# Optimization experiments

Measured on AMD Instinct MI355X. Metric: run time of the kernel, lower is better.

## Reference

```python
import jax, jax.numpy as jnp
import numpy as np

EPS = 1e-6  # LayerNorm eps (added to std, matching torch code)
H = 4       # n_heads
B, D, N, DFF = 8, 512, 1024, 1024


def layer_norm(x, g, b):
    # torch: a_2 * (x - mean) / (std + eps) + b_2, std unbiased (ddof=1)
    m = x.mean(-1, keepdims=True)
    s = x.std(-1, ddof=1, keepdims=True)
    return g * (x - m) / (s + EPS) + b


def mha(q, k, v, W, b):
    # W: [4, d, d] (in->out), b: [4, d]; heads H, d_k = d // H
    Bq, Nq, d = q.shape
    dk = d // H

    def proj(x, i):
        return (x @ W[i] + b[i]).reshape(Bq, -1, H, dk).transpose(0, 2, 1, 3)

    Q, K, V = proj(q, 0), proj(k, 1), proj(v, 2)
    scores = jnp.einsum('bhqd,bhkd->bhqk', Q, K) / np.sqrt(dk).astype(np.float32)
    p = jax.nn.softmax(scores, axis=-1)
    o = jnp.einsum('bhqk,bhkd->bhqd', p, V).transpose(0, 2, 1, 3).reshape(Bq, -1, d)
    return o @ W[3] + b[3]


def ffn(x, w1, b1, w2, b2):
    return jax.nn.relu(x @ w1 + b1) @ w2 + b2


def encoder(x, aw, ab, fw1, fb1, fw2, fb2, lg, lb):
    x = x + mha(layer_norm(x, lg[0], lb[0]), layer_norm(x, lg[0], lb[0]), layer_norm(x, lg[0], lb[0]), aw, ab)
    x = x + ffn(layer_norm(x, lg[1], lb[1]), fw1, fb1, fw2, fb2)
    return layer_norm(x, lg[2], lb[2])


def decoder(x, mem, sw, sb, cw, cb, fw1, fb1, fw2, fb2, lg, lb):
    h0 = layer_norm(x, lg[0], lb[0])
    x = x + mha(h0, h0, h0, sw, sb)
    h1 = layer_norm(x, lg[1], lb[1])
    x = x + mha(h1, mem, mem, cw, cb)
    x = x + ffn(layer_norm(x, lg[2], lb[2]), fw1, fb1, fw2, fb2)
    return layer_norm(x, lg[3], lb[3])


def model(src, tgt, p):
    # src, tgt: [B, N, D]
    mem = encoder(src, p['enc_attn_w'], p['enc_attn_b'], p['enc_ff_w1'], p['enc_ff_b1'],
                  p['enc_ff_w2'], p['enc_ff_b2'], p['enc_ln_g'], p['enc_ln_b'])
    return decoder(tgt, mem, p['dec_sa_w'], p['dec_sa_b'], p['dec_ca_w'], p['dec_ca_b'],
                   p['dec_ff_w1'], p['dec_ff_b1'], p['dec_ff_w2'], p['dec_ff_b2'],
                   p['dec_ln_g'], p['dec_ln_b'])


def setup_inputs() -> dict:
    key = jax.random.key(0)
    ks = jax.random.split(key, 12)
    sc = 0.02
    return {
        'src': jax.random.normal(ks[0], (B, D, N), jnp.float32),
        'tgt': jax.random.normal(ks[1], (B, D, N), jnp.float32),
        'enc_attn_w': jax.random.normal(ks[2], (4, D, D), jnp.float32) * sc,
        'enc_attn_b': jnp.zeros((4, D), jnp.float32),
        'enc_ff_w1': jax.random.normal(ks[3], (D, DFF), jnp.float32) * sc,
        'enc_ff_b1': jnp.zeros((DFF,), jnp.float32),
        'enc_ff_w2': jax.random.normal(ks[4], (DFF, D), jnp.float32) * sc,
        'enc_ff_b2': jnp.zeros((D,), jnp.float32),
        'enc_ln_g': jnp.ones((3, D), jnp.float32),
        'enc_ln_b': jnp.zeros((3, D), jnp.float32),
        'dec_sa_w': jax.random.normal(ks[5], (4, D, D), jnp.float32) * sc,
        'dec_sa_b': jnp.zeros((4, D), jnp.float32),
        'dec_ca_w': jax.random.normal(ks[6], (4, D, D), jnp.float32) * sc,
        'dec_ca_b': jnp.zeros((4, D), jnp.float32),
        'dec_ff_w1': jax.random.normal(ks[7], (D, DFF), jnp.float32) * sc,
        'dec_ff_b1': jnp.zeros((DFF,), jnp.float32),
        'dec_ff_w2': jax.random.normal(ks[8], (DFF, D), jnp.float32) * sc,
        'dec_ff_b2': jnp.zeros((D,), jnp.float32),
        'dec_ln_g': jnp.ones((4, D), jnp.float32),
        'dec_ln_b': jnp.zeros((4, D), jnp.float32),
    }


def reference(src, tgt, enc_attn_w, enc_attn_b, enc_ff_w1, enc_ff_b1, enc_ff_w2, enc_ff_b2,
              enc_ln_g, enc_ln_b, dec_sa_w, dec_sa_b, dec_ca_w, dec_ca_b,
              dec_ff_w1, dec_ff_b1, dec_ff_w2, dec_ff_b2, dec_ln_g, dec_ln_b):
    p = dict(enc_attn_w=enc_attn_w, enc_attn_b=enc_attn_b, enc_ff_w1=enc_ff_w1,
             enc_ff_b1=enc_ff_b1, enc_ff_w2=enc_ff_w2, enc_ff_b2=enc_ff_b2,
             enc_ln_g=enc_ln_g, enc_ln_b=enc_ln_b, dec_sa_w=dec_sa_w, dec_sa_b=dec_sa_b,
             dec_ca_w=dec_ca_w, dec_ca_b=dec_ca_b, dec_ff_w1=dec_ff_w1, dec_ff_b1=dec_ff_b1,
             dec_ff_w2=dec_ff_w2, dec_ff_b2=dec_ff_b2, dec_ln_g=dec_ln_g, dec_ln_b=dec_ln_b)
    s = src.transpose(0, 2, 1)  # [B, N, D]
    t = tgt.transpose(0, 2, 1)
    tgt_embedding = model(s, t, p).transpose(0, 2, 1)  # [B, D, N]
    src_embedding = model(t, s, p).transpose(0, 2, 1)
    return (src_embedding, tgt_embedding)
```

## Files before the change

### kernel.cpp

```cpp
#include <hip/hip_runtime.h>

#define BB 8
#define NN 1024
#define DD 512
#define DFFK 1024
#define HH 4
#define RR (BB * NN)
#define MM (2 * RR)

typedef unsigned short u16;
typedef u16 u16x8 __attribute__((ext_vector_type(8)));
typedef float f32x4 __attribute__((ext_vector_type(4)));
typedef __bf16 bf16x8 __attribute__((ext_vector_type(8)));

__device__ __forceinline__ u16 f32_to_bf16(float f) {
  unsigned int u = __builtin_bit_cast(unsigned int, f);
  unsigned int r = u + 0x7FFFu + ((u >> 16) & 1u);
  return (u16)(r >> 16);
}

__device__ __forceinline__ f32x4 mfma16(u16x8 a, u16x8 b, f32x4 c) {
  return __builtin_amdgcn_mfma_f32_16x16x32_bf16(
      __builtin_bit_cast(bf16x8, a), __builtin_bit_cast(bf16x8, b), c, 0, 0, 0);
}

__device__ __forceinline__ void gl16(u16* lds, const u16* g) {
  __builtin_amdgcn_global_load_lds(
      (const __attribute__((address_space(1))) unsigned int*)g,
      (__attribute__((address_space(3))) unsigned int*)lds, 16, 0, 0);
}

__global__ __launch_bounds__(256) void wconv_kernel(const float* __restrict__ W,
                                                    u16* __restrict__ Wt, int K, int N2, int nmat) {
  int idx = blockIdx.x * 256 + threadIdx.x;
  if (idx >= nmat * K * N2) return;
  int mat = idx / (K * N2), rem = idx % (K * N2);
  int k = rem % K, n = rem / K;
  Wt[(size_t)mat * K * N2 + (size_t)n * K + k] =
      f32_to_bf16(W[(size_t)mat * K * N2 + (size_t)k * N2 + n]);
}

__global__ __launch_bounds__(256) void transpose_kernel(const float* __restrict__ in,
                                                        float* __restrict__ out, int R_, int C_) {
  __shared__ float t[32][33];
  int bx = blockIdx.x * 32, by = blockIdx.y * 32;
  size_t zoff = (size_t)blockIdx.z * R_ * C_;
  const float* ip = in + zoff;
  float* op = out + zoff;
  int tx = threadIdx.x, ty = threadIdx.y;
#pragma unroll
  for (int i = 0; i < 32; i += 8)
    t[ty + i][tx] = ip[(size_t)(by + ty + i) * C_ + bx + tx];
  __syncthreads();
#pragma unroll
  for (int i = 0; i < 32; i += 8)
    op[(size_t)(bx + ty + i) * R_ + by + tx] = t[tx][ty + i];
}

__global__ __launch_bounds__(256) void out_trans_kernel(const float* __restrict__ in,
                                                        float* __restrict__ outA,
                                                        float* __restrict__ outB) {
  __shared__ float t[32][33];
  int z = blockIdx.z;
  int dx = blockIdx.x * 32;
  int sy = blockIdx.y * 32;
  int tx = threadIdx.x, ty = threadIdx.y;
  const float* ip = in + (size_t)z * NN * DD;
#pragma unroll
  for (int i = 0; i < 32; i += 8)
    t[ty + i][tx] = ip[(size_t)(sy + ty + i) * DD + dx + tx];
  __syncthreads();
  float* dst = (z < BB) ? (outA + (size_t)z * DD * NN) : (outB + (size_t)(z - BB) * DD * NN);
#pragma unroll
  for (int i = 0; i < 32; i += 8)
    dst[(size_t)(dx + ty + i) * NN + sy + tx] = t[tx][ty + i];
}

__global__ __launch_bounds__(256) void vtrans_kernel(const u16* __restrict__ V, int vstride,
                                                     u16* __restrict__ Vt) {
  __shared__ u16 t[32][33];
  int z = blockIdx.z;
  int b = z >> 2, h = z & 3;
  int sx = blockIdx.x * 32;
  int dy = blockIdx.y * 32;
  int tx = threadIdx.x, ty = threadIdx.y;
  const u16* ip = V + (size_t)b * NN * vstride + h * 128 + dy;
#pragma unroll
  for (int i = 0; i < 32; i += 8)
    t[ty + i][tx] = ip[(size_t)(sx + ty + i) * vstride + tx];
  __syncthreads();
  u16* op = Vt + ((size_t)z * 128 + dy) * NN + sx;
#pragma unroll
  for (int i = 0; i < 32; i += 8)
    op[(size_t)(ty + i) * NN + tx] = t[tx][ty + i];
}

template <int OUTBF>
__global__ __launch_bounds__(256) void ln_kernel(const float* __restrict__ x0,
                                                 const float* __restrict__ x1,
                                                 const float* __restrict__ g,
                                                 const float* __restrict__ bb,
                                                 void* __restrict__ out) {
  int l = threadIdx.x & 63, w = threadIdx.x >> 6;
  size_t row = (size_t)blockIdx.x * 4 + w;
  const float* xr = (row < RR) ? (x0 + row * DD) : (x1 + (row - RR) * DD);
  float4 v0 = *(const float4*)(xr + l * 8);
  float4 v1 = *(const float4*)(xr + l * 8 + 4);
  float sum = v0.x + v0.y + v0.z + v0.w + v1.x + v1.y + v1.z + v1.w;
  float sq = v0.x * v0.x + v0.y * v0.y + v0.z * v0.z + v0.w * v0.w +
             v1.x * v1.x + v1.y * v1.y + v1.z * v1.z + v1.w * v1.w;
#pragma unroll
  for (int o = 1; o < 64; o <<= 1) {
    sum += __shfl_xor(sum, o);
    sq += __shfl_xor(sq, o);
  }
  float mean = sum * (1.0f / DD);
  float var = fmaxf((sq - (float)DD * mean * mean) * (1.0f / (DD - 1)), 0.0f);
  float inv = 1.0f / (sqrtf(var) + 1e-6f);
  float4 g0 = *(const float4*)(g + l * 8), g1 = *(const float4*)(g + l * 8 + 4);
  float4 b0 = *(const float4*)(bb + l * 8), b1 = *(const float4*)(bb + l * 8 + 4);
  float xs[8] = {v0.x, v0.y, v0.z, v0.w, v1.x, v1.y, v1.z, v1.w};
  float gs[8] = {g0.x, g0.y, g0.z, g0.w, g1.x, g1.y, g1.z, g1.w};
  float bs[8] = {b0.x, b0.y, b0.z, b0.w, b1.x, b1.y, b1.z, b1.w};
  float y[8];
#pragma unroll
  for (int j = 0; j < 8; j++) y[j] = (xs[j] - mean) * inv * gs[j] + bs[j];
  if (OUTBF) {
    u16x8 o8;
#pragma unroll
    for (int j = 0; j < 8; j++) o8[j] = f32_to_bf16(y[j]);
    *(u16x8*)((u16*)out + row * DD + l * 8) = o8;
  } else {
    float4 o0 = {y[0], y[1], y[2], y[3]};
    float4 o1 = {y[4], y[5], y[6], y[7]};
    *(float4*)((float*)out + row * DD + l * 8) = o0;
    *(float4*)((float*)out + row * DD + l * 8 + 4) = o1;
  }
}

template <bool RELU, bool OUT_BF16, bool HAS_RES>
__global__ __launch_bounds__(512) void gemm_bt(const u16* __restrict__ A, int lda,
                                               const u16* __restrict__ Bt,
                                               const float* __restrict__ bias,
                                               const float* res0, const float* res1,
                                               void* Cout, int ldc,
                                               int N2, int Kd) {
  __shared__ u16 sA[2][1024 * 8];
  __shared__ u16 sB[2][512 * 8];
  int tid = threadIdx.x;
  int l = tid & 63, w = tid >> 6;
  int wm = (w >> 1) * 64, wn = (w & 1) * 64;
  int m0 = blockIdx.x * 256, n0 = blockIdx.y * 128;
  f32x4 acc[4][4] = {};

  auto stage = [&](int buf, int k0) {
#pragma unroll
    for (int is = 0; is < 2; is++) {
      int slot = is * 512 + w * 64 + l;
      int chunk = slot >> 8, row = slot & 255;
      gl16(&sA[buf][(size_t)(is * 512 + w * 64) * 8],
           A + (size_t)(m0 + row) * lda + k0 + chunk * 8);
    }
    {
      int slot = w * 64 + l;
      int chunk = slot >> 7, row = slot & 127;
      gl16(&sB[buf][(size_t)(w * 64) * 8],
           Bt + (size_t)(n0 + row) * Kd + k0 + chunk * 8);
    }
  };
  stage(0, 0);
  int buf = 0;
  for (int k0 = 0; k0 < Kd; k0 += 32) {
    __syncthreads();
    if (k0 + 32 < Kd) stage(buf ^ 1, k0 + 32);
    u16x8 af[4], bf[4];
#pragma unroll
    for (int i = 0; i < 4; i++) {
      af[i] = *(const u16x8*)&sA[buf][((l >> 4) * 256 + wm + i * 16 + (l & 15)) * 8];
      bf[i] = *(const u16x8*)&sB[buf][((l >> 4) * 128 + wn + i * 16 + (l & 15)) * 8];
    }
    __builtin_amdgcn_s_setprio(1);
#pragma unroll
    for (int i = 0; i < 4; i++)
#pragma unroll
      for (int j = 0; j < 4; j++) acc[i][j] = mfma16(af[i], bf[j], acc[i][j]);
    __builtin_amdgcn_s_setprio(0);
    buf ^= 1;
  }
  int ccol = l & 15;
  int crow = (l >> 4) * 4;
#pragma unroll
  for (int i = 0; i < 4; i++) {
#pragma unroll
    for (int j = 0; j < 4; j++) {
      int gn = n0 + wn + j * 16 + ccol;
      float bv = bias[gn];
#pragma unroll
      for (int r = 0; r < 4; r++) {
        int gm = m0 + wm + i * 16 + crow + r;
        float v = acc[i][j][r] + bv;
        if (RELU) v = fmaxf(v, 0.0f);
        if (HAS_RES) {
          const float* rp = (gm < RR) ? (res0 + (size_t)gm * DD)
                                      : (res1 + (size_t)(gm - RR) * DD);
          v += rp[gn];
        }
        if (OUT_BF16)
          ((u16*)Cout)[(size_t)gm * ldc + gn] = f32_to_bf16(v);
        else
          ((float*)Cout)[(size_t)gm * ldc + gn] = v;
      }
    }
  }
}

__global__ __launch_bounds__(512, 4) void attn_kernel(const u16* __restrict__ Q, int qstride,
                                                      const u16* __restrict__ K, int kstride,
                                                      const u16* __restrict__ Vt,
                                                      u16* __restrict__ O, int ostride) {
  __shared__ u16 sK[2][64 * 128];
  __shared__ u16 sV[2][128 * 64];
  __shared__ u16 sP[8][16 * 64];
  int tid = threadIdx.x;
  int l = tid & 63, w = tid >> 6;
  int p = blockIdx.x;
  int xcd = p & 7, slot = p >> 3;
  int qb = slot & 7, ghigh = slot >> 3;
  int g = ghigh * 8 + xcd;
  int b = g >> 2, h = g & 3;
  int q0 = qb * 128 + w * 16;
  int bh = g;

  const u16* Qg = Q + (size_t)b * NN * qstride + h * 128;
  const u16* Kg = K + (size_t)b * NN * kstride + h * 128;
  const u16* Vg = Vt + (size_t)bh * 128 * NN;

  u16x8 qf[4];
#pragma unroll
  for (int c = 0; c < 4; c++)
    qf[c] = *(const u16x8*)(Qg + (size_t)(q0 + (l & 15)) * qstride + c * 32 + (l >> 4) * 8);

  f32x4 oacc[8] = {};
  float psum[4] = {0.0f, 0.0f, 0.0f, 0.0f};
  const float scale = 0.08838834764831843f;

  auto stage = [&](int buf, int k0) {
#pragma unroll
    for (int is = 0; is < 2; is++) {
      int slot2 = is * 512 + tid;
      {
        int row = slot2 >> 4, c16 = slot2 & 15;
        int colb = (c16 * 16) ^ ((row & 7) << 4);
        gl16(&sK[buf][(size_t)(is * 512 + w * 64) * 8],
             Kg + (size_t)(k0 + row) * kstride + (colb >> 1));
      }
      {
        int drow = slot2 >> 3, c16 = slot2 & 7;
        int colb = (c16 * 16) ^ ((drow & 7) << 4);
        gl16(&sV[buf][(size_t)(is * 512 + w * 64) * 8],
             Vg + (size_t)drow * NN + k0 + (colb >> 1));
      }
    }
  };

  stage(0, 0);
  int buf = 0;
  for (int t = 0; t < NN / 64; t++) {
    __syncthreads();
    if (t + 1 < NN / 64) stage(buf ^ 1, (t + 1) * 64);
    f32x4 sc[4] = {};
    __builtin_amdgcn_s_setprio(1);
#pragma unroll
    for (int ks = 0; ks < 4; ks++) {
      int row = ks * 16 + (l & 15);
      int swz = (row & 7) << 4;
#pragma unroll
      for (int c = 0; c < 4; c++) {
        int colb = (c * 64 + (l >> 4) * 16) ^ swz;
        u16x8 kf = *(const u16x8*)&sK[buf][row * 128 + (colb >> 1)];
        sc[ks] = mfma16(qf[c], kf, sc[ks]);
      }
    }
    __builtin_amdgcn_s_setprio(0);
#pragma unroll
    for (int r = 0; r < 4; r++) {
      int prow = (l >> 4) * 4 + r;
      int pswz = (prow & 7) << 4;
#pragma unroll
      for (int ks = 0; ks < 4; ks++) {
        float pp = __expf(sc[ks][r] * scale);
        psum[r] += pp;
        int colb = ((ks * 16 + (l & 15)) * 2) ^ pswz;
        sP[w][prow * 64 + (colb >> 1)] = f32_to_bf16(pp);
      }
    }
    u16x8 pf[2];
#pragma unroll
    for (int kc = 0; kc < 2; kc++) {
      int prow = l & 15;
      int colb = (kc * 64 + (l >> 4) * 16) ^ ((prow & 7) << 4);
      pf[kc] = *(const u16x8*)&sP[w][prow * 64 + (colb >> 1)];
    }
    __builtin_amdgcn_s_setprio(1);
#pragma unroll
    for (int n = 0; n < 8; n++) {
      int drow = n * 16 + (l & 15);
      int swz = (drow & 7) << 4;
#pragma unroll
      for (int kc = 0; kc < 2; kc++) {
        int colb = (kc * 64 + (l >> 4) * 16) ^ swz;
        u16x8 vf = *(const u16x8*)&sV[buf][drow * 64 + (colb >> 1)];
        oacc[n] = mfma16(pf[kc], vf, oacc[n]);
      }
    }
    __builtin_amdgcn_s_setprio(0);
    buf ^= 1;
  }
#pragma unroll
  for (int r = 0; r < 4; r++) {
    psum[r] += __shfl_xor(psum[r], 1);
    psum[r] += __shfl_xor(psum[r], 2);
    psum[r] += __shfl_xor(psum[r], 4);
    psum[r] += __shfl_xor(psum[r], 8);
  }
#pragma unroll
  for (int r = 0; r < 4; r++) {
    float inv = 1.0f / psum[r];
    int grow = q0 + (l >> 4) * 4 + r;
    u16* Op = O + ((size_t)b * NN + grow) * ostride + h * 128 + (l & 15);
#pragma unroll
    for (int n = 0; n < 8; n++) Op[n * 16] = f32_to_bf16(oacc[n][r] * inv);
  }
}

extern "C" void kernel_launch(void* const* d_in, const int* in_sizes, int n_in,
                              void* d_out, int out_size, void* d_ws, size_t ws_size,
                              hipStream_t stream) {
  const float* src = (const float*)d_in[0];
  const float* tgt = (const float*)d_in[1];
  const float* enc_attn_w = (const float*)d_in[2];
  const float* enc_attn_b = (const float*)d_in[3];
  const float* enc_ff_w1 = (const float*)d_in[4];
  const float* enc_ff_b1 = (const float*)d_in[5];
  const float* enc_ff_w2 = (const float*)d_in[6];
  const float* enc_ff_b2 = (const float*)d_in[7];
  const float* enc_ln_g = (const float*)d_in[8];
  const float* enc_ln_b = (const float*)d_in[9];
  const float* dec_sa_w = (const float*)d_in[10];
  const float* dec_sa_b = (const float*)d_in[11];
  const float* dec_ca_w = (const float*)d_in[12];
  const float* dec_ca_b = (const float*)d_in[13];
  const float* dec_ff_w1 = (const float*)d_in[14];
  const float* dec_ff_b1 = (const float*)d_in[15];
  const float* dec_ff_w2 = (const float*)d_in[16];
  const float* dec_ff_b2 = (const float*)d_in[17];
  const float* dec_ln_g = (const float*)d_in[18];
  const float* dec_ln_b = (const float*)d_in[19];

  u16* wp = (u16*)d_ws;
  u16* wE = wp;   wp += 4 * DD * DD;
  u16* wS = wp;   wp += 4 * DD * DD;
  u16* wC = wp;   wp += 4 * DD * DD;
  u16* wEff1 = wp; wp += DD * DFFK;
  u16* wEff2 = wp; wp += DD * DFFK;
  u16* wDff1 = wp; wp += DD * DFFK;
  u16* wDff2 = wp; wp += DD * DFFK;
  char* p = (char*)wp;
  float* sT = (float*)p;  p += (size_t)RR * DD * 4;
  float* tT = (float*)p;  p += (size_t)RR * DD * 4;
  float* xb = (float*)p;  p += (size_t)MM * DD * 4;
  u16* hb = (u16*)p;      p += (size_t)MM * DD * 2;
  u16* memb = (u16*)p;    p += (size_t)MM * DD * 2;
  u16* Vt = (u16*)p;      p += (size_t)16 * HH * 128 * NN * 2;
  u16* U = (u16*)p;       p += (size_t)MM * 3 * DD * 2;
  float* xb1 = xb + (size_t)RR * DD;
  float* xtmp = (float*)U;

  wconv_kernel<<<(4 * DD * DD + 255) / 256, 256, 0, stream>>>(enc_attn_w, wE, DD, DD, 4);
  wconv_kernel<<<(4 * DD * DD + 255) / 256, 256, 0, stream>>>(dec_sa_w, wS, DD, DD, 4);
  wconv_kernel<<<(4 * DD * DD + 255) / 256, 256, 0, stream>>>(dec_ca_w, wC, DD, DD, 4);
  wconv_kernel<<<(DD * DFFK + 255) / 256, 256, 0, stream>>>(enc_ff_w1, wEff1, DD, DFFK, 1);
  wconv_kernel<<<(DD * DFFK + 255) / 256, 256, 0, stream>>>(enc_ff_w2, wEff2, DFFK, DD, 1);
  wconv_kernel<<<(DD * DFFK + 255) / 256, 256, 0, stream>>>(dec_ff_w1, wDff1, DD, DFFK, 1);
  wconv_kernel<<<(DD * DFFK + 255) / 256, 256, 0, stream>>>(dec_ff_w2, wDff2, DFFK, DD, 1);

  transpose_kernel<<<dim3(NN / 32, DD / 32, BB), dim3(32, 8), 0, stream>>>(src, sT, DD, NN);
  transpose_kernel<<<dim3(NN / 32, DD / 32, BB), dim3(32, 8), 0, stream>>>(tgt, tT, DD, NN);

  auto ln = [&](const float* x0, const float* x1, const float* g, const float* b,
                void* out, bool bf) {
    if (bf) ln_kernel<1><<<MM / 4, 256, 0, stream>>>(x0, x1, g, b, out);
    else    ln_kernel<0><<<MM / 4, 256, 0, stream>>>(x0, x1, g, b, out);
  };
  auto gemm = [&](const u16* A, int lda, const u16* W, const float* bias,
                  const float* r0, const float* r1, void* out, int ldc,
                  int N2, int K, int mode) {
    dim3 g(MM / 256, N2 / 128);
    if (mode == 0)
      gemm_bt<false, true, false><<<g, 512, 0, stream>>>(A, lda, W, bias, nullptr, nullptr, out, ldc, N2, K);
    else if (mode == 1)
      gemm_bt<true, true, false><<<g, 512, 0, stream>>>(A, lda, W, bias, nullptr, nullptr, out, ldc, N2, K);
    else
      gemm_bt<false, false, true><<<g, 512, 0, stream>>>(A, lda, W, bias, r0, r1, out, ldc, N2, K);
  };
  auto vtrans = [&]() {
    vtrans_kernel<<<dim3(NN / 32, 4, 64), dim3(32, 8), 0, stream>>>(U + 2 * DD, 3 * DD, Vt);
  };
  auto attn = [&]() {
    attn_kernel<<<dim3(512), 512, 0, stream>>>(U, 3 * DD, U + DD, 3 * DD, Vt,
                                               U + 2 * DD, 3 * DD);
  };
  u16* ab = U + 2 * DD;

  ln(sT, tT, enc_ln_g, enc_ln_b, hb, true);
  gemm(hb, DD, wE, enc_attn_b, nullptr, nullptr, U, 3 * DD, 3 * DD, DD, 0);
  vtrans();
  attn();
  gemm(ab, 3 * DD, wE + 3 * DD * DD, enc_attn_b + 3 * DD, sT, tT, xb, DD, DD, DD, 2);
  ln(xb, xb1, enc_ln_g + DD, enc_ln_b + DD, hb, true);
  gemm(hb, DD, wEff1, enc_ff_b1, nullptr, nullptr, U, DFFK, DFFK, DD, 1);
  gemm(U, DFFK, wEff2, enc_ff_b2, xb, xb1, xb, DD, DD, DFFK, 2);
  ln(xb, xb1, enc_ln_g + 2 * DD, enc_ln_b + 2 * DD, memb, true);
  ln(tT, sT, dec_ln_g, dec_ln_b, hb, true);
  gemm(hb, DD, wS, dec_sa_b, nullptr, nullptr, U, 3 * DD, 3 * DD, DD, 0);
  vtrans();
  attn();
  gemm(ab, 3 * DD, wS + 3 * DD * DD, dec_sa_b + 3 * DD, tT, sT, xb, DD, DD, DD, 2);
  ln(xb, xb1, dec_ln_g + DD, dec_ln_b + DD, hb, true);
  gemm(hb, DD, wC, dec_ca_b, nullptr, nullptr, U, 3 * DD, DD, DD, 0);
  gemm(memb, DD, wC + DD * DD, dec_ca_b + DD, nullptr, nullptr, U + DD, 3 * DD,
       2 * DD, DD, 0);
  vtrans();
  attn();
  gemm(ab, 3 * DD, wC + 3 * DD * DD, dec_ca_b + 3 * DD, xb, xb1, xb, DD, DD, DD, 2);
  ln(xb, xb1, dec_ln_g + 2 * DD, dec_ln_b + 2 * DD, hb, true);
  gemm(hb, DD, wDff1, dec_ff_b1, nullptr, nullptr, U, DFFK, DFFK, DD, 1);
  gemm(U, DFFK, wDff2, dec_ff_b2, xb, xb1, xb, DD, DD, DFFK, 2);
  ln(xb, xb1, dec_ln_g + 3 * DD, dec_ln_b + 3 * DD, xtmp, false);
  float* out_f = (float*)d_out;
  out_trans_kernel<<<dim3(DD / 32, NN / 32, 16), dim3(32, 8), 0, stream>>>(
      xtmp, out_f + (size_t)RR * DD, out_f);
}
```

Before: 791.5 us.

## Shrink GEMM tile to 128x128 and stage epilogue through LDS for vector stores

The GEMM block tile shrinks from 256x128 with 512 threads to 128x128 with 256 threads, doubling the grid so more blocks are available to fill the compute units. The epilogue now writes each warp's accumulators to LDS, reads them back transposed, and issues float4 or 4-wide bf16 global stores and float4 residual loads instead of scattered scalar accesses. This is meant to cut uncoalesced epilogue memory traffic. The cost is an extra LDS round trip and barrier at the end, and smaller tiles reload more operand data from global memory.

```diff
diff --git a/kernel.cpp b/kernel.cpp
--- a/kernel.cpp
+++ b/kernel.cpp
@@ -10,6 +10,7 @@
 
 typedef unsigned short u16;
 typedef u16 u16x8 __attribute__((ext_vector_type(8)));
+typedef u16 u16x4 __attribute__((ext_vector_type(4)));
 typedef float f32x4 __attribute__((ext_vector_type(4)));
 typedef __bf16 bf16x8 __attribute__((ext_vector_type(8)));
 
@@ -139,32 +140,28 @@
 }
 
 template <bool RELU, bool OUT_BF16, bool HAS_RES>
-__global__ __launch_bounds__(512) void gemm_bt(const u16* __restrict__ A, int lda,
+__global__ __launch_bounds__(256) void gemm_bt(const u16* __restrict__ A, int lda,
                                                const u16* __restrict__ Bt,
                                                const float* __restrict__ bias,
                                                const float* res0, const float* res1,
                                                void* Cout, int ldc,
                                                int N2, int Kd) {
-  __shared__ u16 sA[2][1024 * 8];
+  __shared__ u16 sA[2][512 * 8];
   __shared__ u16 sB[2][512 * 8];
   int tid = threadIdx.x;
   int l = tid & 63, w = tid >> 6;
   int wm = (w >> 1) * 64, wn = (w & 1) * 64;
-  int m0 = blockIdx.x * 256, n0 = blockIdx.y * 128;
+  int m0 = blockIdx.x * 128, n0 = blockIdx.y * 128;
   f32x4 acc[4][4] = {};
 
   auto stage = [&](int buf, int k0) {
 #pragma unroll
     for (int is = 0; is < 2; is++) {
-      int slot = is * 512 + w * 64 + l;
-      int chunk = slot >> 8, row = slot & 255;
-      gl16(&sA[buf][(size_t)(is * 512 + w * 64) * 8],
+      int slot = is * 256 + w * 64 + l;
+      int chunk = slot >> 7, row = slot & 127;
+      gl16(&sA[buf][(size_t)(is * 256 + w * 64) * 8],
            A + (size_t)(m0 + row) * lda + k0 + chunk * 8);
-    }
-    {
-      int slot = w * 64 + l;
-      int chunk = slot >> 7, row = slot & 127;
-      gl16(&sB[buf][(size_t)(w * 64) * 8],
+      gl16(&sB[buf][(size_t)(is * 256 + w * 64) * 8],
            Bt + (size_t)(n0 + row) * Kd + k0 + chunk * 8);
     }
   };
@@ -176,7 +173,7 @@
     u16x8 af[4], bf[4];
 #pragma unroll
     for (int i = 0; i < 4; i++) {
-      af[i] = *(const u16x8*)&sA[buf][((l >> 4) * 256 + wm + i * 16 + (l & 15)) * 8];
+      af[i] = *(const u16x8*)&sA[buf][((l >> 4) * 128 + wm + i * 16 + (l & 15)) * 8];
       bf[i] = *(const u16x8*)&sB[buf][((l >> 4) * 128 + wn + i * 16 + (l & 15)) * 8];
     }
     __builtin_amdgcn_s_setprio(1);
@@ -187,28 +184,41 @@
     __builtin_amdgcn_s_setprio(0);
     buf ^= 1;
   }
-  int ccol = l & 15;
-  int crow = (l >> 4) * 4;
+  __syncthreads();
+  float* eTw = (float*)&sA[0][0] + w * 1024;
+  float4 bias4 = *(const float4*)&bias[n0 + wn + (l & 15) * 4];
 #pragma unroll
   for (int i = 0; i < 4; i++) {
 #pragma unroll
-    for (int j = 0; j < 4; j++) {
-      int gn = n0 + wn + j * 16 + ccol;
-      float bv = bias[gn];
-#pragma unroll
-      for (int r = 0; r < 4; r++) {
-        int gm = m0 + wm + i * 16 + crow + r;
-        float v = acc[i][j][r] + bv;
-        if (RELU) v = fmaxf(v, 0.0f);
-        if (HAS_RES) {
-          const float* rp = (gm < RR) ? (res0 + (size_t)gm * DD)
-                                      : (res1 + (size_t)(gm - RR) * DD);
-          v += rp[gn];
-        }
-        if (OUT_BF16)
-          ((u16*)Cout)[(size_t)gm * ldc + gn] = f32_to_bf16(v);
-        else
-          ((float*)Cout)[(size_t)gm * ldc + gn] = v;
+    for (int j = 0; j < 4; j++)
+#pragma unroll
+      for (int r = 0; r < 4; r++)
+        eTw[((l >> 4) * 4 + r) * 64 + j * 16 + (l & 15)] = acc[i][j][r];
+#pragma unroll
+    for (int t = 0; t < 4; t++) {
+      int row = t * 4 + (l >> 4);
+      int f4 = l & 15;
+      float4 v4 = *(float4*)&eTw[row * 64 + f4 * 4];
+      int gm = m0 + wm + i * 16 + row;
+      int gn = n0 + wn + f4 * 4;
+      v4.x += bias4.x; v4.y += bias4.y; v4.z += bias4.z; v4.w += bias4.w;
+      if (RELU) {
+        v4.x = fmaxf(v4.x, 0.0f); v4.y = fmaxf(v4.y, 0.0f);
+        v4.z = fmaxf(v4.z, 0.0f); v4.w = fmaxf(v4.w, 0.0f);
+      }
+      if (HAS_RES) {
+        const float* rp = (gm < RR) ? (res0 + (size_t)gm * DD)
+                                    : (res1 + (size_t)(gm - RR) * DD);
+        float4 r4 = *(const float4*)&rp[gn];
+        v4.x += r4.x; v4.y += r4.y; v4.z += r4.z; v4.w += r4.w;
+      }
+      if (OUT_BF16) {
+        u16x4 o4;
+        o4[0] = f32_to_bf16(v4.x); o4[1] = f32_to_bf16(v4.y);
+        o4[2] = f32_to_bf16(v4.z); o4[3] = f32_to_bf16(v4.w);
+        *(u16x4*)&((u16*)Cout)[(size_t)gm * ldc + gn] = o4;
+      } else {
+        *(float4*)&((float*)Cout)[(size_t)gm * ldc + gn] = v4;
       }
     }
   }
@@ -395,13 +405,13 @@
   auto gemm = [&](const u16* A, int lda, const u16* W, const float* bias,
                   const float* r0, const float* r1, void* out, int ldc,
                   int N2, int K, int mode) {
-    dim3 g(MM / 256, N2 / 128);
+    dim3 g(MM / 128, N2 / 128);
     if (mode == 0)
-      gemm_bt<false, true, false><<<g, 512, 0, stream>>>(A, lda, W, bias, nullptr, nullptr, out, ldc, N2, K);
+      gemm_bt<false, true, false><<<g, 256, 0, stream>>>(A, lda, W, bias, nullptr, nullptr, out, ldc, N2, K);
     else if (mode == 1)
-      gemm_bt<true, true, false><<<g, 512, 0, stream>>>(A, lda, W, bias, nullptr, nullptr, out, ldc, N2, K);
+      gemm_bt<true, true, false><<<g, 256, 0, stream>>>(A, lda, W, bias, nullptr, nullptr, out, ldc, N2, K);
     else
-      gemm_bt<false, false, true><<<g, 512, 0, stream>>>(A, lda, W, bias, r0, r1, out, ldc, N2, K);
+      gemm_bt<false, false, true><<<g, 256, 0, stream>>>(A, lda, W, bias, r0, r1, out, ldc, N2, K);
   };
   auto vtrans = [&]() {
     vtrans_kernel<<<dim3(NN / 32, 4, 64), dim3(32, 8), 0, stream>>>(U + 2 * DD, 3 * DD, Vt);
```

Measured after the change: 735.3 us. 7.1% less time.
